# Kernel tuning notes

Measured on AMD Instinct MI355X. Metric: run time of the kernel, lower is better.

Reference implementation:

```python
import jax, jax.numpy as jnp
import numpy as np

SIGMA_SQ = 0.01  # sigma=0.1
EPS = 1e-20      # sqrt(EPS)=1e-10 matches the module's distance clamp


def setup_inputs() -> dict:
    key = jax.random.key(0)
    ks = jax.random.split(key, 9)
    M, L, N, d, H = 4, 8, 512, 2, 32
    data = jax.random.normal(ks[0], (M, L, N, d), dtype=jnp.float32)
    t_snapshots = jnp.arange(L, dtype=jnp.float32)  # increasing times -> dt=1
    W1 = jax.random.normal(ks[1], (d, H), dtype=jnp.float32) * 0.5
    b1 = jax.random.normal(ks[2], (H,), dtype=jnp.float32) * 0.1
    w2 = jax.random.normal(ks[3], (H,), dtype=jnp.float32) * 0.5
    b2 = jax.random.normal(ks[4], (1,), dtype=jnp.float32) * 0.1
    p1 = jax.random.normal(ks[5], (H,), dtype=jnp.float32) * 0.5
    pb1 = jax.random.normal(ks[6], (H,), dtype=jnp.float32) * 0.1
    p2 = jax.random.normal(ks[7], (H,), dtype=jnp.float32) * 0.5
    pb2 = jax.random.normal(ks[8], (1,), dtype=jnp.float32) * 0.1
    return {"data": data, "t_snapshots": t_snapshots, "W1": W1, "b1": b1,
            "w2": w2, "b2": b2, "p1": p1, "pb1": pb1, "p2": p2, "pb2": pb2}


def reference(data, t_snapshots, W1, b1, w2, b2, p1, pb1, p2, pb2):
    M, L, N, d = data.shape
    mask = 1.0 - jnp.eye(N, dtype=data.dtype)  # zero out diagonal (i == j)

    def v_terms(X):
        # V(x) = w2 . tanh(W1^T x + b1) + b2 ; analytic grad and Laplacian
        t = jnp.tanh(X @ W1 + b1)                      # (N, H)
        s = 1.0 - t * t                                # sech^2
        V = t @ w2 + b2[0]                             # (N,)
        gV = (s * w2) @ W1.T                           # (N, d)
        lapV = (-2.0 * t * s * w2) @ (W1 * W1).sum(0)  # (N,)
        return V, gV, lapV

    def pdist(X):
        diff = X[:, None, :] - X[None, :, :]           # (N, N, d)
        sq = (diff * diff).sum(-1)
        dist = jnp.sqrt(jnp.maximum(sq, EPS))          # diag -> 1e-10 (== clamp)
        return diff, dist

    def phi_terms(dist):
        # Phi(r) = p2 . tanh(p1 r + pb1) + pb2 ; analytic dPhi/dr, d2Phi/dr2
        t = jnp.tanh(dist[..., None] * p1 + pb1)       # (N, N, H)
        s = 1.0 - t * t
        Phi = t @ p2 + pb2[0]                          # (N, N)
        dPhi = (s * p1) @ p2                           # (N, N)
        d2Phi = (-2.0 * t * s * (p1 * p1)) @ p2        # (N, N)
        return Phi, dPhi, d2Phi

    def energy(X):
        V, _, _ = v_terms(X)
        _, dist = pdist(X)
        Phi = jnp.tanh(dist[..., None] * p1 + pb1) @ p2 + pb2[0]
        return V.mean() + (Phi * mask).sum() / (N * N)

    def step(carry, inp):
        Xc, Xn, dt = inp
        V, gV, lapV = v_terms(Xc)
        diff, dist = pdist(Xc)
        Phi, dPhi, d2Phi = phi_terms(dist)
        # drift_i = -grad_V(X_i) - (1/N) sum_j dPhi(r_ij) * (X_i - X_j)/r_ij
        unit = diff / dist[..., None]
        gPhi_mean = ((dPhi * mask)[..., None] * unit).sum(1) / N   # (N, d)
        drift = -gV - gPhi_mean
        J_diss = (drift * drift).sum() / N * dt
        # Laplacian of radial Phi in d dims: d2Phi + (d-1)/r * dPhi
        lapPhi = d2Phi + (d - 1) / dist * dPhi
        lap_sum = lapV + (lapPhi * mask).sum(1) / N                # (N,)
        J_diff = SIGMA_SQ * lap_sum.mean() * dt
        E_curr = V.mean() + (Phi * mask).sum() / (N * N)
        dE = energy(Xn) - E_curr
        return carry + jnp.stack([J_diss, J_diff, dE]), None

    S = M * (L - 1)
    Xc_all = data[:, :-1].reshape(S, N, d)
    Xn_all = data[:, 1:].reshape(S, N, d)
    dts = jnp.tile(t_snapshots[1:] - t_snapshots[:-1], M)          # (S,)
    totals, _ = jax.lax.scan(step, jnp.zeros(3, data.dtype), (Xc_all, Xn_all, dts))
    totals = totals / S
    residual = totals[0] + totals[1] - 2.0 * totals[2]
    return residual * residual
```

## Files before the change

### kernel.cpp

```cpp
#include <hip/hip_runtime.h>

#define N_PART 512
#define H_DIM 32
#define M_DIM 4
#define L_DIM 8
#define N_STEPS (M_DIM * (L_DIM - 1))
#define N_JOBS (N_STEPS + M_DIM)
#define NBLK (N_JOBS * 32)
#define NCELL 2048
#define RMAX 10.0f
#define TSCALE ((float)NCELL / RMAX)
#define TWO_LOG2E 2.8853900817779268f

#define TAB_FLOATS (NCELL * 3)
#define TAB_BYTES (TAB_FLOATS * 4)
#define ST_OFF TAB_BYTES
#define ST_BYTES (NCELL * 4)
#define PART_OFF (TAB_BYTES + ST_BYTES)

__global__ __launch_bounds__(256)
void tfl_tabgen(const float* __restrict__ p1, const float* __restrict__ pb1,
                const float* __restrict__ p2, float* __restrict__ tab,
                float* __restrict__ stTab) {
  const int c = blockIdx.x * 256 + threadIdx.x;
  if (c >= NCELL) return;
  const float r = (float)c * (RMAX / (float)NCELL);
  float St = 0.f, Sg = 0.f, Sl = 0.f;
  for (int h = 0; h < H_DIM; ++h) {
    float p1h = p1[h], P2h = p2[h];
    float arg = TWO_LOG2E * fmaf(r, p1h, pb1[h]);
    float y = __builtin_amdgcn_exp2f(arg);
    float u = __builtin_amdgcn_rcpf(y + 1.0f);
    float t = fmaf(-2.0f, u, 1.0f);
    float dd = fmaf(-u, u, u);
    St = fmaf(t, P2h, St);
    Sg = fmaf(dd, 4.0f * p1h * P2h, Sg);
    Sl = fmaf(t * dd, -8.0f * p1h * p1h * P2h, Sl);
  }
  tab[3 * c + 0] = St;
  tab[3 * c + 1] = Sg;
  tab[3 * c + 2] = Sl;
  stTab[c] = St;
}

__global__ __launch_bounds__(512)
void tfl_main8(const float* __restrict__ data, const float* __restrict__ tsnap,
               const float* __restrict__ W1, const float* __restrict__ b1,
               const float* __restrict__ w2, const float* __restrict__ tab,
               const float* __restrict__ stTab, double* __restrict__ partials) {
  const int jb = blockIdx.x >> 5;
  const int rb = blockIdx.x & 31;
  const bool emode = (jb >= N_STEPS);
  const int m = emode ? (jb - N_STEPS) : jb / (L_DIM - 1);
  const int l = emode ? (L_DIM - 1) : jb % (L_DIM - 1);
  const bool l0 = (!emode && l == 0);
  const float* X = data + (size_t)(m * L_DIM + l) * (N_PART * 2);

  __shared__ __align__(16) float sTab[TAB_FLOATS];
  __shared__ __align__(16) float Xs[N_PART * 2];
  __shared__ double sred[8][3];

  const int tid = threadIdx.x;
  if (tid < 256) ((float4*)Xs)[tid] = ((const float4*)X)[tid];
  if (!emode) {
#pragma unroll
    for (int q = 0; q < 3; ++q)
      ((float4*)sTab)[tid + 512 * q] = ((const float4*)tab)[tid + 512 * q];
  } else {
    ((float4*)sTab)[tid] = ((const float4*)stTab)[tid];
  }
  __syncthreads();

  const int wv = tid >> 6;
  const int ln = tid & 63;
  const int g = ln & 31;
  const int row = rb * 16 + (tid >> 5);
  const float xi0 = Xs[2 * row], xi1 = Xs[2 * row + 1];
  const float invN = 1.0f / N_PART;
  const float invN2 = invN * invN;
  const float rs0 = __builtin_amdgcn_rsqf(1e-20f);
  const float2* Xs2 = (const float2*)Xs;

  float bJd = 0.f, bLap = 0.f, bE = 0.f;

  if (!emode && !l0) {
    float aGx = 0.f, aGy = 0.f, aLw = 0.f;
#pragma unroll 4
    for (int kk = 0; kk < 16; ++kk) {
      const int j = g + 32 * kk;
      float2 xj = Xs2[j];
      float dx = xi0 - xj.x, dy = xi1 - xj.y;
      float sq = fmaxf(fmaf(dx, dx, dy * dy), 1e-20f);
      float rs = __builtin_amdgcn_rsqf(sq);
      float r = sq * rs;
      int ki = (int)fmaf(r, TSCALE, 0.5f);
      ki = min(ki, NCELL - 1);
      const int b = 3 * ki;
      float Sgv = sTab[b + 1], Slv = sTab[b + 2];
      float tg = Sgv * rs;
      aGx = fmaf(dx, tg, aGx);
      aGy = fmaf(dy, tg, aGy);
      aLw += tg + Slv;
    }
    float gVx, gVy, lapV;
    {
      float w10 = W1[g], w11 = W1[H_DIM + g], w2h = w2[g];
      float arg = TWO_LOG2E * fmaf(xi0, w10, fmaf(xi1, w11, b1[g]));
      float y = __builtin_amdgcn_exp2f(arg);
      float u = __builtin_amdgcn_rcpf(y + 1.0f);
      float t = fmaf(-2.0f, u, 1.0f);
      float dd = fmaf(-u, u, u);
      float g4 = 4.0f * dd * w2h;
      gVx = g4 * w10;
      gVy = g4 * w11;
      lapV = t * dd * (-8.0f * w2h) * fmaf(w10, w10, w11 * w11);
    }
    float gx = fmaf(aGx, invN, gVx);
    float gy = fmaf(aGy, invN, gVy);
    float lw = fmaf(aLw, invN, lapV);
#pragma unroll
    for (int sh = 1; sh < 32; sh <<= 1) {
      gx += __shfl_xor(gx, sh);
      gy += __shfl_xor(gy, sh);
      lw += __shfl_xor(lw, sh);
    }
    lw -= fmaf(sTab[1], rs0, sTab[2]) * invN;
    float cJd = fmaf(gx, gx, gy * gy);
    cJd += __shfl_xor(cJd, 32);
    lw += __shfl_xor(lw, 32);
    bJd = cJd; bLap = lw;
  } else if (l0) {
    float aSt = 0.f, aGx = 0.f, aGy = 0.f, aLw = 0.f;
#pragma unroll 4
    for (int kk = 0; kk < 16; ++kk) {
      const int j = g + 32 * kk;
      float2 xj = Xs2[j];
      float dx = xi0 - xj.x, dy = xi1 - xj.y;
      float sq = fmaxf(fmaf(dx, dx, dy * dy), 1e-20f);
      float rs = __builtin_amdgcn_rsqf(sq);
      float r = sq * rs;
      int ki = (int)fmaf(r, TSCALE, 0.5f);
      ki = min(ki, NCELL - 1);
      const int b = 3 * ki;
      float Stv = sTab[b], Sgv = sTab[b + 1], Slv = sTab[b + 2];
      float tg = Sgv * rs;
      aSt += Stv;
      aGx = fmaf(dx, tg, aGx);
      aGy = fmaf(dy, tg, aGy);
      aLw += tg + Slv;
    }
    float Vi, gVx, gVy, lapV;
    {
      float w10 = W1[g], w11 = W1[H_DIM + g], w2h = w2[g];
      float arg = TWO_LOG2E * fmaf(xi0, w10, fmaf(xi1, w11, b1[g]));
      float y = __builtin_amdgcn_exp2f(arg);
      float u = __builtin_amdgcn_rcpf(y + 1.0f);
      float t = fmaf(-2.0f, u, 1.0f);
      float dd = fmaf(-u, u, u);
      Vi = t * w2h;
      float g4 = 4.0f * dd * w2h;
      gVx = g4 * w10;
      gVy = g4 * w11;
      lapV = t * dd * (-8.0f * w2h) * fmaf(w10, w10, w11 * w11);
    }
    float eA = fmaf(aSt, invN2, Vi * invN);
    float gx = fmaf(aGx, invN, gVx);
    float gy = fmaf(aGy, invN, gVy);
    float lw = fmaf(aLw, invN, lapV);
#pragma unroll
    for (int sh = 1; sh < 32; sh <<= 1) {
      eA += __shfl_xor(eA, sh);
      gx += __shfl_xor(gx, sh);
      gy += __shfl_xor(gy, sh);
      lw += __shfl_xor(lw, sh);
    }
    eA -= sTab[0] * invN2;
    lw -= fmaf(sTab[1], rs0, sTab[2]) * invN;
    float cJd = fmaf(gx, gx, gy * gy);
    cJd += __shfl_xor(cJd, 32);
    lw += __shfl_xor(lw, 32);
    eA += __shfl_xor(eA, 32);
    bJd = cJd; bLap = lw; bE = eA;
  } else {
    float aSt = 0.f;
#pragma unroll 4
    for (int kk = 0; kk < 16; ++kk) {
      const int j = g + 32 * kk;
      float2 xj = Xs2[j];
      float dx = xi0 - xj.x, dy = xi1 - xj.y;
      float sq = fmaxf(fmaf(dx, dx, dy * dy), 1e-20f);
      float rs = __builtin_amdgcn_rsqf(sq);
      float r = sq * rs;
      int ki = (int)fmaf(r, TSCALE, 0.5f);
      ki = min(ki, NCELL - 1);
      aSt += sTab[ki];
    }
    float Vi;
    {
      float w10 = W1[g], w11 = W1[H_DIM + g], w2h = w2[g];
      float arg = TWO_LOG2E * fmaf(xi0, w10, fmaf(xi1, w11, b1[g]));
      float y = __builtin_amdgcn_exp2f(arg);
      float u = __builtin_amdgcn_rcpf(y + 1.0f);
      float t = fmaf(-2.0f, u, 1.0f);
      Vi = t * w2h;
    }
    float eA = fmaf(aSt, invN2, Vi * invN);
#pragma unroll
    for (int sh = 1; sh < 32; sh <<= 1) eA += __shfl_xor(eA, sh);
    eA -= sTab[0] * invN2;
    eA += __shfl_xor(eA, 32);
    bE = eA;
  }

  if (ln == 0) { sred[wv][0] = bJd; sred[wv][1] = bLap; sred[wv][2] = bE; }
  __syncthreads();
  if (tid == 0) {
    double sJd = 0, sLap = 0, sE = 0;
    for (int w = 0; w < 8; ++w) {
      sJd += sred[w][0]; sLap += sred[w][1]; sE += sred[w][2];
    }
    const double dN = 1.0 / N_PART;
    double j0 = 0.0, j1 = 0.0, j2 = 0.0;
    if (emode) {
      j2 = sE;
    } else {
      double dt = (double)(tsnap[l + 1] - tsnap[l]);
      j0 = dt * dN * sJd;
      j1 = dt * 0.01 * dN * sLap;
      if (l == 0) j2 = -sE;
    }
    partials[(size_t)blockIdx.x * 3 + 0] = j0;
    partials[(size_t)blockIdx.x * 3 + 1] = j1;
    partials[(size_t)blockIdx.x * 3 + 2] = j2;
  }
}

__global__ __launch_bounds__(512)
void tfl_finalize(const double* __restrict__ partials, float* __restrict__ out) {
  __shared__ double sred[8][3];
  const int tid = threadIdx.x;
  const int wv = tid >> 6;
  const int ln = tid & 63;
  const double* pa = partials + (size_t)tid * 3;
  const double* pb = partials + (size_t)(tid + 512) * 3;
  double t0 = pa[0] + pb[0];
  double t1 = pa[1] + pb[1];
  double t2 = pa[2] + pb[2];
#pragma unroll
  for (int sh = 1; sh < 64; sh <<= 1) {
    t0 += __shfl_xor(t0, sh);
    t1 += __shfl_xor(t1, sh);
    t2 += __shfl_xor(t2, sh);
  }
  if (ln == 0) { sred[wv][0] = t0; sred[wv][1] = t1; sred[wv][2] = t2; }
  __syncthreads();
  if (tid == 0) {
    double s0 = 0, s1 = 0, s2 = 0;
    for (int w = 0; w < 8; ++w) {
      s0 += sred[w][0]; s1 += sred[w][1]; s2 += sred[w][2];
    }
    double r = (s0 + s1 - 2.0 * s2) / (double)N_STEPS;
    out[0] = (float)(r * r);
  }
}

extern "C" void kernel_launch(void* const* d_in, const int* in_sizes, int n_in,
                              void* d_out, int out_size, void* d_ws, size_t ws_size,
                              hipStream_t stream) {
  (void)in_sizes; (void)n_in; (void)out_size; (void)ws_size;
  const float* data  = (const float*)d_in[0];
  const float* tsnap = (const float*)d_in[1];
  const float* W1    = (const float*)d_in[2];
  const float* b1    = (const float*)d_in[3];
  const float* w2    = (const float*)d_in[4];
  const float* p1    = (const float*)d_in[6];
  const float* pb1   = (const float*)d_in[7];
  const float* p2    = (const float*)d_in[8];
  float* tab = (float*)d_ws;
  float* stTab = (float*)((char*)d_ws + ST_OFF);
  double* partials = (double*)((char*)d_ws + PART_OFF);
  float* out = (float*)d_out;

  hipLaunchKernelGGL(tfl_tabgen, dim3(NCELL / 256), dim3(256), 0, stream,
                     p1, pb1, p2, tab, stTab);
  hipLaunchKernelGGL(tfl_main8, dim3(NBLK), dim3(512), 0, stream,
                     data, tsnap, W1, b1, w2, tab, stTab, partials);
  hipLaunchKernelGGL(tfl_finalize, dim3(1), dim3(512), 0, stream, partials, out);
}
```

Baseline: 20.89 us.

## Split potential table into planes and use 1024-thread blocks with fewer blocks

Stores the St/Sg/Sl lookup tables as three separate planes instead of an interleaved triple, so each block copies only the planes its mode needs into shared memory (Sg+Sl for drift steps, all three for l=0, St only for energy jobs). Blocks grow to 1024 threads covering 32 rows, which halves the block count and the number of per-block table loads. The finalize kernel is simplified to read one partial per thread. Larger blocks may lower scheduling flexibility and occupancy per CU.

```diff
diff --git a/kernel.cpp b/kernel.cpp
--- a/kernel.cpp
+++ b/kernel.cpp
@@ -6,22 +6,23 @@
 #define L_DIM 8
 #define N_STEPS (M_DIM * (L_DIM - 1))
 #define N_JOBS (N_STEPS + M_DIM)
-#define NBLK (N_JOBS * 32)
+#define BLK_PER_JOB 16
+#define NBLK (N_JOBS * BLK_PER_JOB)
 #define NCELL 2048
 #define RMAX 10.0f
 #define TSCALE ((float)NCELL / RMAX)
 #define TWO_LOG2E 2.8853900817779268f
 
-#define TAB_FLOATS (NCELL * 3)
-#define TAB_BYTES (TAB_FLOATS * 4)
-#define ST_OFF TAB_BYTES
-#define ST_BYTES (NCELL * 4)
-#define PART_OFF (TAB_BYTES + ST_BYTES)
+#define PLANE_FLOATS NCELL
+#define ST_OFF 0
+#define SG_OFF (NCELL * 4)
+#define SL_OFF (NCELL * 8)
+#define PART_OFF (NCELL * 12)
 
 __global__ __launch_bounds__(256)
 void tfl_tabgen(const float* __restrict__ p1, const float* __restrict__ pb1,
-                const float* __restrict__ p2, float* __restrict__ tab,
-                float* __restrict__ stTab) {
+                const float* __restrict__ p2, float* __restrict__ stTab,
+                float* __restrict__ sgTab, float* __restrict__ slTab) {
   const int c = blockIdx.x * 256 + threadIdx.x;
   if (c >= NCELL) return;
   const float r = (float)c * (RMAX / (float)NCELL);
@@ -37,44 +38,49 @@
     Sg = fmaf(dd, 4.0f * p1h * P2h, Sg);
     Sl = fmaf(t * dd, -8.0f * p1h * p1h * P2h, Sl);
   }
-  tab[3 * c + 0] = St;
-  tab[3 * c + 1] = Sg;
-  tab[3 * c + 2] = Sl;
   stTab[c] = St;
-}
-
-__global__ __launch_bounds__(512)
-void tfl_main8(const float* __restrict__ data, const float* __restrict__ tsnap,
-               const float* __restrict__ W1, const float* __restrict__ b1,
-               const float* __restrict__ w2, const float* __restrict__ tab,
-               const float* __restrict__ stTab, double* __restrict__ partials) {
-  const int jb = blockIdx.x >> 5;
-  const int rb = blockIdx.x & 31;
+  sgTab[c] = Sg;
+  slTab[c] = Sl;
+}
+
+__global__ __launch_bounds__(1024)
+void tfl_main10(const float* __restrict__ data, const float* __restrict__ tsnap,
+                const float* __restrict__ W1, const float* __restrict__ b1,
+                const float* __restrict__ w2, const float* __restrict__ tabAll,
+                double* __restrict__ partials) {
+  const int jb = blockIdx.x >> 4;
+  const int rb = blockIdx.x & 15;
   const bool emode = (jb >= N_STEPS);
   const int m = emode ? (jb - N_STEPS) : jb / (L_DIM - 1);
   const int l = emode ? (L_DIM - 1) : jb % (L_DIM - 1);
   const bool l0 = (!emode && l == 0);
   const float* X = data + (size_t)(m * L_DIM + l) * (N_PART * 2);
 
-  __shared__ __align__(16) float sTab[TAB_FLOATS];
+  __shared__ __align__(16) float sPl[NCELL * 3];
   __shared__ __align__(16) float Xs[N_PART * 2];
-  __shared__ double sred[8][3];
+  __shared__ double sred[16][3];
+
+  float* const sSt = sPl;
+  float* const sSg = sPl + NCELL;
+  float* const sSl = sPl + 2 * NCELL;
 
   const int tid = threadIdx.x;
   if (tid < 256) ((float4*)Xs)[tid] = ((const float4*)X)[tid];
-  if (!emode) {
-#pragma unroll
-    for (int q = 0; q < 3; ++q)
-      ((float4*)sTab)[tid + 512 * q] = ((const float4*)tab)[tid + 512 * q];
+  if (!emode && !l0) {
+    ((float4*)sPl)[512 + tid] = ((const float4*)tabAll)[512 + tid];
+  } else if (l0) {
+    ((float4*)sPl)[tid] = ((const float4*)tabAll)[tid];
+    if (tid < 512)
+      ((float4*)sPl)[1024 + tid] = ((const float4*)tabAll)[1024 + tid];
   } else {
-    ((float4*)sTab)[tid] = ((const float4*)stTab)[tid];
+    if (tid < 512) ((float4*)sPl)[tid] = ((const float4*)tabAll)[tid];
   }
   __syncthreads();
 
   const int wv = tid >> 6;
   const int ln = tid & 63;
   const int g = ln & 31;
-  const int row = rb * 16 + (tid >> 5);
+  const int row = rb * 32 + (tid >> 5);
   const float xi0 = Xs[2 * row], xi1 = Xs[2 * row + 1];
   const float invN = 1.0f / N_PART;
   const float invN2 = invN * invN;
@@ -95,8 +101,7 @@
       float r = sq * rs;
       int ki = (int)fmaf(r, TSCALE, 0.5f);
       ki = min(ki, NCELL - 1);
-      const int b = 3 * ki;
-      float Sgv = sTab[b + 1], Slv = sTab[b + 2];
+      float Sgv = sSg[ki], Slv = sSl[ki];
       float tg = Sgv * rs;
       aGx = fmaf(dx, tg, aGx);
       aGy = fmaf(dy, tg, aGy);
@@ -124,7 +129,7 @@
       gy += __shfl_xor(gy, sh);
       lw += __shfl_xor(lw, sh);
     }
-    lw -= fmaf(sTab[1], rs0, sTab[2]) * invN;
+    lw -= fmaf(sSg[0], rs0, sSl[0]) * invN;
     float cJd = fmaf(gx, gx, gy * gy);
     cJd += __shfl_xor(cJd, 32);
     lw += __shfl_xor(lw, 32);
@@ -141,8 +146,7 @@
       float r = sq * rs;
       int ki = (int)fmaf(r, TSCALE, 0.5f);
       ki = min(ki, NCELL - 1);
-      const int b = 3 * ki;
-      float Stv = sTab[b], Sgv = sTab[b + 1], Slv = sTab[b + 2];
+      float Stv = sSt[ki], Sgv = sSg[ki], Slv = sSl[ki];
       float tg = Sgv * rs;
       aSt += Stv;
       aGx = fmaf(dx, tg, aGx);
@@ -174,8 +178,8 @@
       gy += __shfl_xor(gy, sh);
       lw += __shfl_xor(lw, sh);
     }
-    eA -= sTab[0] * invN2;
-    lw -= fmaf(sTab[1], rs0, sTab[2]) * invN;
+    eA -= sSt[0] * invN2;
+    lw -= fmaf(sSg[0], rs0, sSl[0]) * invN;
     float cJd = fmaf(gx, gx, gy * gy);
     cJd += __shfl_xor(cJd, 32);
     lw += __shfl_xor(lw, 32);
@@ -193,7 +197,7 @@
       float r = sq * rs;
       int ki = (int)fmaf(r, TSCALE, 0.5f);
       ki = min(ki, NCELL - 1);
-      aSt += sTab[ki];
+      aSt += sSt[ki];
     }
     float Vi;
     {
@@ -207,7 +211,7 @@
     float eA = fmaf(aSt, invN2, Vi * invN);
 #pragma unroll
     for (int sh = 1; sh < 32; sh <<= 1) eA += __shfl_xor(eA, sh);
-    eA -= sTab[0] * invN2;
+    eA -= sSt[0] * invN2;
     eA += __shfl_xor(eA, 32);
     bE = eA;
   }
@@ -216,7 +220,7 @@
   __syncthreads();
   if (tid == 0) {
     double sJd = 0, sLap = 0, sE = 0;
-    for (int w = 0; w < 8; ++w) {
+    for (int w = 0; w < 16; ++w) {
       sJd += sred[w][0]; sLap += sred[w][1]; sE += sred[w][2];
     }
     const double dN = 1.0 / N_PART;
@@ -242,10 +246,7 @@
   const int wv = tid >> 6;
   const int ln = tid & 63;
   const double* pa = partials + (size_t)tid * 3;
-  const double* pb = partials + (size_t)(tid + 512) * 3;
-  double t0 = pa[0] + pb[0];
-  double t1 = pa[1] + pb[1];
-  double t2 = pa[2] + pb[2];
+  double t0 = pa[0], t1 = pa[1], t2 = pa[2];
 #pragma unroll
   for (int sh = 1; sh < 64; sh <<= 1) {
     t0 += __shfl_xor(t0, sh);
@@ -276,14 +277,16 @@
   const float* p1    = (const float*)d_in[6];
   const float* pb1   = (const float*)d_in[7];
   const float* p2    = (const float*)d_in[8];
-  float* tab = (float*)d_ws;
+  float* tabAll = (float*)d_ws;
   float* stTab = (float*)((char*)d_ws + ST_OFF);
+  float* sgTab = (float*)((char*)d_ws + SG_OFF);
+  float* slTab = (float*)((char*)d_ws + SL_OFF);
   double* partials = (double*)((char*)d_ws + PART_OFF);
   float* out = (float*)d_out;
 
   hipLaunchKernelGGL(tfl_tabgen, dim3(NCELL / 256), dim3(256), 0, stream,
-                     p1, pb1, p2, tab, stTab);
-  hipLaunchKernelGGL(tfl_main8, dim3(NBLK), dim3(512), 0, stream,
-                     data, tsnap, W1, b1, w2, tab, stTab, partials);
+                     p1, pb1, p2, stTab, sgTab, slTab);
+  hipLaunchKernelGGL(tfl_main10, dim3(NBLK), dim3(1024), 0, stream,
+                     data, tsnap, W1, b1, w2, tabAll, partials);
   hipLaunchKernelGGL(tfl_finalize, dim3(1), dim3(512), 0, stream, partials, out);
 }
```

After: 20.95 us. Within noise of the previous version (+0.3%).
